# Performance work log

Hardware: AMD Instinct MI355X
Metric: run time of the kernel (lower is better)

Reference implementation:

```python
import jax, jax.numpy as jnp
import numpy as np

DIM = 128
POS_HID = 64
ATTN_MULT = 4
K_NEIGH = 16
B, N = 2, 2048


def setup_inputs() -> dict:
    key = jax.random.key(0)
    ks = jax.random.split(key, 10)
    s = 0.02
    inp = {
        "x": jax.random.normal(ks[0], (B, N, DIM), dtype=jnp.float32),
        "pos": jax.random.normal(ks[1], (B, N, 3), dtype=jnp.float32),
        "mask": jnp.ones((B, N), dtype=bool),
        # to_qkv: Linear(dim, 3*dim, bias=False) -> W (3*dim, dim)
        "Wqkv": jax.random.normal(ks[2], (3 * DIM, DIM), dtype=jnp.float32) * s,
        # pos_mlp: Linear(3, 64) -> ReLU -> Linear(64, dim)
        "Wp1": jax.random.normal(ks[3], (POS_HID, 3), dtype=jnp.float32) * s,
        "bp1": jnp.zeros((POS_HID,), dtype=jnp.float32),
        "Wp2": jax.random.normal(ks[4], (DIM, POS_HID), dtype=jnp.float32) * s,
        "bp2": jnp.zeros((DIM,), dtype=jnp.float32),
        # attn_mlp: Linear(dim, 4*dim) -> ReLU -> Linear(4*dim, dim)
        "Wa1": jax.random.normal(ks[5], (ATTN_MULT * DIM, DIM), dtype=jnp.float32) * s,
        "ba1": jnp.zeros((ATTN_MULT * DIM,), dtype=jnp.float32),
        "Wa2": jax.random.normal(ks[6], (DIM, ATTN_MULT * DIM), dtype=jnp.float32) * s,
        "ba2": jnp.zeros((DIM,), dtype=jnp.float32),
    }
    return inp


def _forward(x, pos, mask, Wqkv, Wp1, bp1, Wp2, bp2, Wa1, ba1, Wa2, ba2):
    b, n, d = x.shape
    qkv = jnp.einsum("bnd,ed->bne", x, Wqkv)  # (b, n, 3*dim)
    q, k, v = jnp.split(qkv, 3, axis=-1)

    # pairwise distances over full n x n for kNN selection
    rel_pos_full = pos[:, :, None, :] - pos[:, None, :, :]  # (b, n, n, 3)
    rel_dist = jnp.linalg.norm(rel_pos_full, axis=-1)        # (b, n, n)
    pair_mask = mask[:, :, None] & mask[:, None, :]
    big = jnp.finfo(rel_dist.dtype).max
    rel_dist = jnp.where(pair_mask, rel_dist, big)

    # topk smallest distances -> neighbor indices (b, n, K)
    _, idx = jax.lax.top_k(-rel_dist, K_NEIGH)

    bi = jnp.arange(b)[:, None, None]
    k_g = k[bi, idx]      # (b, n, K, dim)
    v_g = v[bi, idx]      # (b, n, K, dim)
    pos_g = pos[bi, idx]  # (b, n, K, 3)
    mask_g = jnp.take_along_axis(pair_mask, idx, axis=2)  # (b, n, K)

    # relative position embedding (computed on gathered neighbors; same math
    # as applying pos_mlp on the full n x n tensor then gathering)
    rel_pos = pos[:, :, None, :] - pos_g  # (b, n, K, 3)
    h = jax.nn.relu(jnp.einsum("bnkc,hc->bnkh", rel_pos, Wp1) + bp1)
    rel_pos_emb = jnp.einsum("bnkh,dh->bnkd", h, Wp2) + bp2  # (b, n, K, dim)

    qk_rel = q[:, :, None, :] - k_g  # (b, n, K, dim)
    v_g = v_g + rel_pos_emb

    a = jax.nn.relu(jnp.einsum("bnkd,hd->bnkh", qk_rel + rel_pos_emb, Wa1) + ba1)
    sim = jnp.einsum("bnkh,dh->bnkd", a, Wa2) + ba2  # (b, n, K, dim)

    neg_big = -jnp.finfo(sim.dtype).max
    sim = jnp.where(mask_g[..., None], sim, neg_big)
    attn = jax.nn.softmax(sim, axis=-2)  # softmax over neighbors
    agg = jnp.sum(attn * v_g, axis=2)    # (b, n, dim)
    return agg


def reference(x, pos, mask, Wqkv, Wp1, bp1, Wp2, bp2, Wa1, ba1, Wa2, ba2):
    return _forward(x, pos, mask, Wqkv, Wp1, bp1, Wp2, bp2, Wa1, ba1, Wa2, ba2)
```

## Files before the change

kernel.cpp:

```cpp
#include <hip/hip_runtime.h>
#include <float.h>

#define DIM   128
#define PH    64
#define AH    512
#define KN    16
#define BATCH 2
#define NPTS  2048
#define QB    4
#define RWS   64
#define HC    64
#define NCH   (AH/HC)
#define QR    8
#define KNB   8
#define KBUF  48

#define NB_KNN  (BATCH*NPTS/KNB)
#define NB_QKV  (BATCH*NPTS/QR)
#define NB_CONV 544

typedef __attribute__((ext_vector_type(8))) short bf16x8;
typedef __attribute__((ext_vector_type(4))) float f32x4;

__device__ __forceinline__ unsigned short f2bf(float f) {
    unsigned u = __float_as_uint(f);
    u += 0x7FFFu + ((u >> 16) & 1u);
    return (unsigned short)(u >> 16);
}
__device__ __forceinline__ float bfu(unsigned short u) {
    return __uint_as_float((unsigned)u << 16);
}

__device__ __forceinline__ int yoff(int row, int col) {
    return row * 128 + ((((col >> 3) ^ (row & 7)) << 3) | (col & 7));
}
__device__ __forceinline__ int hoff(int row, int col) {
    return row * 64 + ((((col >> 3) ^ (row & 7)) << 3) | (col & 7));
}

__device__ __forceinline__ unsigned long long bitonic64(unsigned long long key, int lane) {
    #pragma unroll
    for (int k = 2; k <= 64; k <<= 1) {
        #pragma unroll
        for (int j = k >> 1; j > 0; j >>= 1) {
            unsigned long long o = __shfl_xor(key, j);
            bool up  = ((lane & k) == 0);
            bool low = ((lane & j) == 0);
            unsigned long long mn = key < o ? key : o;
            unsigned long long mx = key < o ? o : key;
            key = (up == low) ? mn : mx;
        }
    }
    return key;
}

__device__ __forceinline__ void topk_step(
    unsigned long long key, bool active,
    unsigned long long& lkey, unsigned long long& kmax,
    int& base, unsigned long long* bufw, int lane) {
    unsigned long long m = __ballot(active);
    while (m) {
        int space = KBUF - base;
        int rank  = __popcll(m & ((1ull << lane) - 1ull));
        bool mine = (m >> lane) & 1ull;
        bool app  = mine && (rank < space);
        if (app) bufw[base + rank] = key;
        int cnt = __popcll(m);
        if (cnt <= space) { base += cnt; break; }
        unsigned long long k2 = (lane < KN) ? lkey : bufw[lane - KN];
        k2   = bitonic64(k2, lane);
        lkey = (lane < KN) ? k2 : ~0ull;
        kmax = __shfl(k2, 15);
        base = 0;
        active = active && !app && (key < kmax);
        m = __ballot(active);
    }
}

__global__ __launch_bounds__(256) void front_kernel(
    const float* __restrict__ x, const float* __restrict__ pos,
    const float* __restrict__ Wqkv,
    const float* __restrict__ Wa1, const float* __restrict__ Wa2,
    const float* __restrict__ Wp2,
    float* __restrict__ qkv, int* __restrict__ knn,
    unsigned short* __restrict__ Wa1b, unsigned short* __restrict__ Wa2b,
    unsigned short* __restrict__ Wp2b) {

    __shared__ __align__(16) unsigned char smem[3 * NPTS * 4 + KNB * KBUF * 8];
    int bid = blockIdx.x;
    int t   = threadIdx.x;

    if (bid < NB_KNN) {
        float* lin = (float*)smem;
        unsigned long long (*buf)[KBUF] =
            (unsigned long long(*)[KBUF])(smem + 3 * NPTS * 4);

        int lane = t & 63;
        int wv   = t >> 6;
        int q0   = bid * KNB;
        int b    = q0 >> 11;

        const float* pb = pos + (size_t)b * NPTS * 3;
        for (int i = t; i < 3 * NPTS; i += 256)
            lin[i] = pb[i];
        __syncthreads();

        int qA  = q0 + wv * 2 + 0;
        int qB  = q0 + wv * 2 + 1;
        int iA  = qA & (NPTS - 1), iB = qB & (NPTS - 1);
        float qxA = lin[3 * iA + 0], qyA = lin[3 * iA + 1], qzA = lin[3 * iA + 2];
        float qxB = lin[3 * iB + 0], qyB = lin[3 * iB + 1], qzB = lin[3 * iB + 2];

        unsigned long long lkeyA, lkeyB;
        {
            float cx = lin[3 * lane + 0], cy = lin[3 * lane + 1], cz = lin[3 * lane + 2];
            float dxA = qxA - cx, dyA = qyA - cy, dzA = qzA - cz;
            float dxB = qxB - cx, dyB = qyB - cy, dzB = qzB - cz;
            float d2A = dxA * dxA + dyA * dyA + dzA * dzA;
            float d2B = dxB * dxB + dyB * dyB + dzB * dzB;
            unsigned long long kA =
                ((unsigned long long)__float_as_uint(d2A) << 32) | (unsigned)lane;
            unsigned long long kB =
                ((unsigned long long)__float_as_uint(d2B) << 32) | (unsigned)lane;
            kA = bitonic64(kA, lane);
            kB = bitonic64(kB, lane);
            lkeyA = (lane < KN) ? kA : ~0ull;
            lkeyB = (lane < KN) ? kB : ~0ull;
        }
        unsigned long long kmaxA = __shfl(lkeyA, 15);
        unsigned long long kmaxB = __shfl(lkeyB, 15);
        int baseA = 0, baseB = 0;
        unsigned long long* bufA = buf[wv * 2 + 0];
        unsigned long long* bufB = buf[wv * 2 + 1];

        for (int c = 1; c < NPTS / 64; c++) {
            int j = c * 64 + lane;
            float cx = lin[3 * j + 0], cy = lin[3 * j + 1], cz = lin[3 * j + 2];
            float dxA = qxA - cx, dyA = qyA - cy, dzA = qzA - cz;
            float dxB = qxB - cx, dyB = qyB - cy, dzB = qzB - cz;
            float d2A = dxA * dxA + dyA * dyA + dzA * dzA;
            float d2B = dxB * dxB + dyB * dyB + dzB * dzB;
            unsigned long long kA =
                ((unsigned long long)__float_as_uint(d2A) << 32) | (unsigned)j;
            unsigned long long kB =
                ((unsigned long long)__float_as_uint(d2B) << 32) | (unsigned)j;
            topk_step(kA, kA < kmaxA, lkeyA, kmaxA, baseA, bufA, lane);
            topk_step(kB, kB < kmaxB, lkeyB, kmaxB, baseB, bufB, lane);
        }
        if (baseA) {
            unsigned long long k2 = (lane < KN) ? lkeyA
                : ((lane - KN < baseA) ? bufA[lane - KN] : ~0ull);
            lkeyA = bitonic64(k2, lane);
        }
        if (baseB) {
            unsigned long long k2 = (lane < KN) ? lkeyB
                : ((lane - KN < baseB) ? bufB[lane - KN] : ~0ull);
            lkeyB = bitonic64(k2, lane);
        }
        if (lane < KN) {
            knn[qA * KN + lane] = (int)(unsigned)(lkeyA & 0xFFFFFFFFull);
            knn[qB * KN + lane] = (int)(unsigned)(lkeyB & 0xFFFFFFFFull);
        }
        return;
    }

    if (bid < NB_KNN + NB_QKV) {
        int r0 = (bid - NB_KNN) * QR;
        float (*xr)[DIM] = (float(*)[DIM])smem;
        for (int i = t; i < QR * DIM; i += 256)
            xr[i >> 7][i & 127] = x[(size_t)(r0 + (i >> 7)) * DIM + (i & 127)];
        __syncthreads();
        for (int e = t; e < 3 * DIM; e += 256) {
            const float* wp = Wqkv + e * DIM;
            float a[QR];
            #pragma unroll
            for (int r = 0; r < QR; r++) a[r] = 0.f;
            for (int d = 0; d < DIM; d += 4) {
                float4 wv = *(const float4*)(wp + d);
                #pragma unroll
                for (int r = 0; r < QR; r++) {
                    float4 xv = *(const float4*)&xr[r][d];
                    a[r] += xv.x * wv.x + xv.y * wv.y + xv.z * wv.z + xv.w * wv.w;
                }
            }
            #pragma unroll
            for (int r = 0; r < QR; r++)
                qkv[(size_t)(r0 + r) * 3 * DIM + e] = a[r];
        }
        return;
    }

    {
        int i = (bid - NB_KNN - NB_QKV) * 256 + t;
        if (i < AH * DIM) Wa1b[i] = f2bf(Wa1[i]);
        else if (i < 2 * AH * DIM) Wa2b[i - AH * DIM] = f2bf(Wa2[i - AH * DIM]);
        else if (i < 2 * AH * DIM + DIM * PH) Wp2b[i - 2 * AH * DIM] = f2bf(Wp2[i - 2 * AH * DIM]);
    }
}

__global__ __launch_bounds__(256, 4) void fused_kernel(
    const float* __restrict__ qkv, const float* __restrict__ pos,
    const int* __restrict__ knn,
    const float* __restrict__ Wp1, const float* __restrict__ bp1,
    const float* __restrict__ bp2,
    const unsigned short* __restrict__ Wp2b,
    const unsigned short* __restrict__ Wa1b, const float* __restrict__ ba1,
    const unsigned short* __restrict__ Wa2b, const float* __restrict__ ba2,
    float* __restrict__ out) {

    __shared__ __align__(16) unsigned short Yl[RWS * DIM];
    __shared__ __align__(16) unsigned short Bl[RWS * HC];
    __shared__ __align__(16) unsigned short Vl[RWS * DIM];

    float* qf   = (float*)Bl;
    int*   nid  = (int*)Bl + 512;
    float* relp = (float*)Bl + 576;
    unsigned short* Hh = Vl;

    int t  = threadIdx.x;
    int bid = blockIdx.x;
    int x8 = bid & 7, n8 = bid >> 3;
    int jq = (x8 >> 2) * 512 + n8 * 4 + (x8 & 3);
    int q0 = jq * QB;
    int gb = q0 >> 11;

    for (int i = t; i < QB * DIM; i += 256)
        qf[i] = qkv[(size_t)(q0 + (i >> 7)) * 3 * DIM + (i & 127)];
    if (t < RWS) nid[t] = knn[q0 * KN + t];
    __syncthreads();
    if (t < RWS) {
        int gq = q0 + (t >> 4);
        int gn = (gb << 11) + nid[t];
        relp[t * 3 + 0] = pos[gq * 3 + 0] - pos[gn * 3 + 0];
        relp[t * 3 + 1] = pos[gq * 3 + 1] - pos[gn * 3 + 1];
        relp[t * 3 + 2] = pos[gq * 3 + 2] - pos[gn * 3 + 2];
    }
    __syncthreads();

    for (int i = t; i < RWS * PH; i += 256) {
        int row = i >> 6, h = i & 63;
        float hv = relp[row * 3 + 0] * Wp1[h * 3 + 0]
                 + relp[row * 3 + 1] * Wp1[h * 3 + 1]
                 + relp[row * 3 + 2] * Wp1[h * 3 + 2] + bp1[h];
        Hh[hoff(row, h)] = f2bf(fmaxf(hv, 0.f));
    }
    __syncthreads();

    int w = t >> 6, lane = t & 63, lg = lane >> 4, lr = lane & 15;

    f32x4 emb[4][2];
    #pragma unroll
    for (int mi = 0; mi < 4; mi++)
        #pragma unroll
        for (int ni = 0; ni < 2; ni++) {
            float bz = bp2[w * 32 + ni * 16 + lr];
            emb[mi][ni] = (f32x4){bz, bz, bz, bz};
        }
    #pragma unroll
    for (int kk = 0; kk < 2; kk++) {
        bf16x8 bfr[2];
        #pragma unroll
        for (int ni = 0; ni < 2; ni++)
            bfr[ni] = *(const bf16x8*)(Wp2b + (w * 32 + ni * 16 + lr) * PH + kk * 32 + lg * 8);
        #pragma unroll
        for (int mi = 0; mi < 4; mi++) {
            bf16x8 afr = *(const bf16x8*)&Hh[hoff(mi * 16 + lr, kk * 32 + lg * 8)];
            #pragma unroll
            for (int ni = 0; ni < 2; ni++)
                emb[mi][ni] = __builtin_amdgcn_mfma_f32_16x16x32_bf16(afr, bfr[ni], emb[mi][ni], 0, 0, 0);
        }
    }

    #pragma unroll
    for (int mi = 0; mi < 4; mi++)
        #pragma unroll
        for (int ni = 0; ni < 2; ni++) {
            int colb = w * 32 + ni * 16 + lr;
            #pragma unroll
            for (int r = 0; r < 4; r++)
                Yl[yoff(mi * 16 + lg * 4 + r, colb)] = f2bf(emb[mi][ni][r]);
        }
    __syncthreads();

    for (int i = t; i < RWS * 32; i += 256) {
        int row = i >> 5, cg = (i & 31) * 4;
        const float* kvp = qkv + (size_t)((gb << 11) + nid[row]) * 3 * DIM;
        float4 kg = *(const float4*)(kvp + DIM + cg);
        float4 vg = *(const float4*)(kvp + 2 * DIM + cg);
        float4 qv = *(const float4*)(qf + (row >> 4) * DIM + cg);
        int off = yoff(row, cg);
        ushort4 em = *(const ushort4*)&Yl[off];
        float e0 = bfu(em.x), e1 = bfu(em.y), e2 = bfu(em.z), e3 = bfu(em.w);
        ushort4 yv, vv;
        yv.x = f2bf(qv.x - kg.x + e0); yv.y = f2bf(qv.y - kg.y + e1);
        yv.z = f2bf(qv.z - kg.z + e2); yv.w = f2bf(qv.w - kg.w + e3);
        vv.x = f2bf(vg.x + e0); vv.y = f2bf(vg.y + e1);
        vv.z = f2bf(vg.z + e2); vv.w = f2bf(vg.w + e3);
        *(ushort4*)&Yl[off] = yv;
        *(ushort4*)&Vl[off] = vv;
    }
    __syncthreads();

    f32x4 sim[4][2];
    #pragma unroll
    for (int mi = 0; mi < 4; mi++)
        #pragma unroll
        for (int ni = 0; ni < 2; ni++) {
            float bz = ba2[w * 32 + ni * 16 + lr];
            sim[mi][ni] = (f32x4){bz, bz, bz, bz};
        }

    #pragma unroll 2
    for (int ch = 0; ch < NCH; ch++) {
        bf16x8 w1f[4], w2f[4];
        #pragma unroll
        for (int kk = 0; kk < 4; kk++)
            w1f[kk] = *(const bf16x8*)(Wa1b + (ch * HC + w * 16 + lr) * DIM + kk * 32 + lg * 8);
        #pragma unroll
        for (int i = 0; i < 4; i++) {
            int kk = i >> 1, ni = i & 1;
            w2f[i] = *(const bf16x8*)(Wa2b + (w * 32 + ni * 16 + lr) * AH + ch * HC + kk * 32 + lg * 8);
        }

        f32x4 ac[4];
        float bz = ba1[ch * HC + w * 16 + lr];
        #pragma unroll
        for (int mi = 0; mi < 4; mi++) ac[mi] = (f32x4){bz, bz, bz, bz};
        #pragma unroll
        for (int kk = 0; kk < 4; kk++)
            #pragma unroll
            for (int mi = 0; mi < 4; mi++) {
                bf16x8 afr = *(const bf16x8*)&Yl[yoff(mi * 16 + lr, kk * 32 + lg * 8)];
                ac[mi] = __builtin_amdgcn_mfma_f32_16x16x32_bf16(afr, w1f[kk], ac[mi], 0, 0, 0);
            }
        #pragma unroll
        for (int mi = 0; mi < 4; mi++)
            #pragma unroll
            for (int r = 0; r < 4; r++)
                Bl[hoff(mi * 16 + lg * 4 + r, w * 16 + lr)] = f2bf(fmaxf(ac[mi][r], 0.f));
        __syncthreads();

        #pragma unroll
        for (int kk = 0; kk < 2; kk++)
            #pragma unroll
            for (int mi = 0; mi < 4; mi++) {
                bf16x8 afr = *(const bf16x8*)&Bl[hoff(mi * 16 + lr, kk * 32 + lg * 8)];
                #pragma unroll
                for (int ni = 0; ni < 2; ni++)
                    sim[mi][ni] = __builtin_amdgcn_mfma_f32_16x16x32_bf16(afr, w2f[kk * 2 + ni], sim[mi][ni], 0, 0, 0);
            }
        __syncthreads();
    }

    #pragma unroll
    for (int mi = 0; mi < 4; mi++) {
        #pragma unroll
        for (int ni = 0; ni < 2; ni++) {
            int colb = w * 32 + ni * 16 + lr;
            int rw   = mi * 16 + lg * 4;
            float s0 = sim[mi][ni][0], s1 = sim[mi][ni][1];
            float s2 = sim[mi][ni][2], s3 = sim[mi][ni][3];
            float m = fmaxf(fmaxf(s0, s1), fmaxf(s2, s3));
            m = fmaxf(m, __shfl_xor(m, 16));
            m = fmaxf(m, __shfl_xor(m, 32));
            float e0 = __expf(s0 - m), e1 = __expf(s1 - m);
            float e2 = __expf(s2 - m), e3 = __expf(s3 - m);
            float v0 = bfu(Vl[yoff(rw + 0, colb)]);
            float v1 = bfu(Vl[yoff(rw + 1, colb)]);
            float v2 = bfu(Vl[yoff(rw + 2, colb)]);
            float v3 = bfu(Vl[yoff(rw + 3, colb)]);
            float ssum = (e0 + e1) + (e2 + e3);
            float wsum = (e0 * v0 + e1 * v1) + (e2 * v2 + e3 * v3);
            ssum += __shfl_xor(ssum, 16);
            ssum += __shfl_xor(ssum, 32);
            wsum += __shfl_xor(wsum, 16);
            wsum += __shfl_xor(wsum, 32);
            if (lg == 0)
                out[(size_t)(q0 + mi) * DIM + colb] = wsum / ssum;
        }
    }
}

extern "C" void kernel_launch(void* const* d_in, const int* in_sizes, int n_in,
                              void* d_out, int out_size, void* d_ws, size_t ws_size,
                              hipStream_t stream) {
    const float* x    = (const float*)d_in[0];
    const float* pos  = (const float*)d_in[1];
    const float* Wqkv = (const float*)d_in[3];
    const float* Wp1  = (const float*)d_in[4];
    const float* bp1  = (const float*)d_in[5];
    const float* Wp2  = (const float*)d_in[6];
    const float* bp2  = (const float*)d_in[7];
    const float* Wa1  = (const float*)d_in[8];
    const float* ba1  = (const float*)d_in[9];
    const float* Wa2  = (const float*)d_in[10];
    const float* ba2  = (const float*)d_in[11];
    float* out = (float*)d_out;

    char* ws = (char*)d_ws;
    float* qkv = (float*)ws;                              ws += (size_t)BATCH * NPTS * 3 * DIM * 4;
    int*   knn = (int*)ws;                                ws += (size_t)BATCH * NPTS * KN * 4;
    unsigned short* Wa1b = (unsigned short*)ws;           ws += AH * DIM * 2;
    unsigned short* Wa2b = (unsigned short*)ws;           ws += AH * DIM * 2;
    unsigned short* Wp2b = (unsigned short*)ws;           ws += DIM * PH * 2;

    front_kernel<<<NB_KNN + NB_QKV + NB_CONV, 256, 0, stream>>>(
        x, pos, Wqkv, Wa1, Wa2, Wp2, qkv, knn, Wa1b, Wa2b, Wp2b);
    fused_kernel<<<BATCH * NPTS / QB, 256, 0, stream>>>(qkv, pos, knn,
                                                        Wp1, bp1, bp2, Wp2b,
                                                        Wa1b, ba1, Wa2b, ba2, out);
}
```

Measured before the change: 78.49 us.

## Partition attention MLP by query rows per wave, removing block barriers

Each wave now owns one query's 16 neighbor rows and computes the full hidden and output width for them, instead of all waves splitting the output columns across all rows. The Y fragments are kept in registers, and the Bl hidden tile is written and read only by the same wave, so both __syncthreads per chunk go away. The cost is that every wave loads the whole Wa1/Wa2 chunk itself, so per-wave weight traffic from global/L2 rises, and sim accumulators grow to 8 tiles per wave.

Result: slower. 155.4 us (+98.1%).

```diff
diff --git a/kernel.cpp b/kernel.cpp
--- a/kernel.cpp
+++ b/kernel.cpp
@@ -301,83 +301,76 @@
     }
     __syncthreads();
 
-    f32x4 sim[4][2];
-    #pragma unroll
-    for (int mi = 0; mi < 4; mi++)
-        #pragma unroll
-        for (int ni = 0; ni < 2; ni++) {
-            float bz = ba2[w * 32 + ni * 16 + lr];
-            sim[mi][ni] = (f32x4){bz, bz, bz, bz};
-        }
-
-    #pragma unroll 2
+    bf16x8 yreg[4];
+    #pragma unroll
+    for (int kk = 0; kk < 4; kk++)
+        yreg[kk] = *(const bf16x8*)&Yl[yoff(w * 16 + lr, kk * 32 + lg * 8)];
+
+    f32x4 sim[8];
+    #pragma unroll
+    for (int ni = 0; ni < 8; ni++) {
+        float bz = ba2[ni * 16 + lr];
+        sim[ni] = (f32x4){bz, bz, bz, bz};
+    }
+
     for (int ch = 0; ch < NCH; ch++) {
-        bf16x8 w1f[4], w2f[4];
-        #pragma unroll
-        for (int kk = 0; kk < 4; kk++)
-            w1f[kk] = *(const bf16x8*)(Wa1b + (ch * HC + w * 16 + lr) * DIM + kk * 32 + lg * 8);
-        #pragma unroll
-        for (int i = 0; i < 4; i++) {
-            int kk = i >> 1, ni = i & 1;
-            w2f[i] = *(const bf16x8*)(Wa2b + (w * 32 + ni * 16 + lr) * AH + ch * HC + kk * 32 + lg * 8);
-        }
-
         f32x4 ac[4];
-        float bz = ba1[ch * HC + w * 16 + lr];
-        #pragma unroll
-        for (int mi = 0; mi < 4; mi++) ac[mi] = (f32x4){bz, bz, bz, bz};
-        #pragma unroll
-        for (int kk = 0; kk < 4; kk++)
-            #pragma unroll
-            for (int mi = 0; mi < 4; mi++) {
-                bf16x8 afr = *(const bf16x8*)&Yl[yoff(mi * 16 + lr, kk * 32 + lg * 8)];
-                ac[mi] = __builtin_amdgcn_mfma_f32_16x16x32_bf16(afr, w1f[kk], ac[mi], 0, 0, 0);
+        #pragma unroll
+        for (int ni = 0; ni < 4; ni++) {
+            float b1 = ba1[ch * HC + ni * 16 + lr];
+            ac[ni] = (f32x4){b1, b1, b1, b1};
+        }
+        #pragma unroll
+        for (int kk = 0; kk < 4; kk++) {
+            bf16x8 w1a = *(const bf16x8*)(Wa1b + (size_t)(ch * HC + 0 * 16 + lr) * DIM + kk * 32 + lg * 8);
+            bf16x8 w1b = *(const bf16x8*)(Wa1b + (size_t)(ch * HC + 1 * 16 + lr) * DIM + kk * 32 + lg * 8);
+            bf16x8 w1c = *(const bf16x8*)(Wa1b + (size_t)(ch * HC + 2 * 16 + lr) * DIM + kk * 32 + lg * 8);
+            bf16x8 w1d = *(const bf16x8*)(Wa1b + (size_t)(ch * HC + 3 * 16 + lr) * DIM + kk * 32 + lg * 8);
+            ac[0] = __builtin_amdgcn_mfma_f32_16x16x32_bf16(yreg[kk], w1a, ac[0], 0, 0, 0);
+            ac[1] = __builtin_amdgcn_mfma_f32_16x16x32_bf16(yreg[kk], w1b, ac[1], 0, 0, 0);
+            ac[2] = __builtin_amdgcn_mfma_f32_16x16x32_bf16(yreg[kk], w1c, ac[2], 0, 0, 0);
+            ac[3] = __builtin_amdgcn_mfma_f32_16x16x32_bf16(yreg[kk], w1d, ac[3], 0, 0, 0);
+        }
+        #pragma unroll
+        for (int ni = 0; ni < 4; ni++)
+            #pragma unroll
+            for (int r = 0; r < 4; r++)
+                Bl[hoff(w * 16 + lg * 4 + r, ni * 16 + lr)] = f2bf(fmaxf(ac[ni][r], 0.f));
+
+        #pragma unroll
+        for (int kk = 0; kk < 2; kk++) {
+            bf16x8 afr = *(const bf16x8*)&Bl[hoff(w * 16 + lr, kk * 32 + lg * 8)];
+            #pragma unroll
+            for (int ni = 0; ni < 8; ni++) {
+                bf16x8 w2 = *(const bf16x8*)(Wa2b + (size_t)(ni * 16 + lr) * AH + ch * HC + kk * 32 + lg * 8);
+                sim[ni] = __builtin_amdgcn_mfma_f32_16x16x32_bf16(afr, w2, sim[ni], 0, 0, 0);
             }
-        #pragma unroll
-        for (int mi = 0; mi < 4; mi++)
-            #pragma unroll
-            for (int r = 0; r < 4; r++)
-                Bl[hoff(mi * 16 + lg * 4 + r, w * 16 + lr)] = f2bf(fmaxf(ac[mi][r], 0.f));
-        __syncthreads();
-
-        #pragma unroll
-        for (int kk = 0; kk < 2; kk++)
-            #pragma unroll
-            for (int mi = 0; mi < 4; mi++) {
-                bf16x8 afr = *(const bf16x8*)&Bl[hoff(mi * 16 + lr, kk * 32 + lg * 8)];
-                #pragma unroll
-                for (int ni = 0; ni < 2; ni++)
-                    sim[mi][ni] = __builtin_amdgcn_mfma_f32_16x16x32_bf16(afr, w2f[kk * 2 + ni], sim[mi][ni], 0, 0, 0);
-            }
-        __syncthreads();
-    }
-
-    #pragma unroll
-    for (int mi = 0; mi < 4; mi++) {
-        #pragma unroll
-        for (int ni = 0; ni < 2; ni++) {
-            int colb = w * 32 + ni * 16 + lr;
-            int rw   = mi * 16 + lg * 4;
-            float s0 = sim[mi][ni][0], s1 = sim[mi][ni][1];
-            float s2 = sim[mi][ni][2], s3 = sim[mi][ni][3];
-            float m = fmaxf(fmaxf(s0, s1), fmaxf(s2, s3));
-            m = fmaxf(m, __shfl_xor(m, 16));
-            m = fmaxf(m, __shfl_xor(m, 32));
-            float e0 = __expf(s0 - m), e1 = __expf(s1 - m);
-            float e2 = __expf(s2 - m), e3 = __expf(s3 - m);
-            float v0 = bfu(Vl[yoff(rw + 0, colb)]);
-            float v1 = bfu(Vl[yoff(rw + 1, colb)]);
-            float v2 = bfu(Vl[yoff(rw + 2, colb)]);
-            float v3 = bfu(Vl[yoff(rw + 3, colb)]);
-            float ssum = (e0 + e1) + (e2 + e3);
-            float wsum = (e0 * v0 + e1 * v1) + (e2 * v2 + e3 * v3);
-            ssum += __shfl_xor(ssum, 16);
-            ssum += __shfl_xor(ssum, 32);
-            wsum += __shfl_xor(wsum, 16);
-            wsum += __shfl_xor(wsum, 32);
-            if (lg == 0)
-                out[(size_t)(q0 + mi) * DIM + colb] = wsum / ssum;
-        }
+        }
+    }
+
+    #pragma unroll
+    for (int ni = 0; ni < 8; ni++) {
+        int colb = ni * 16 + lr;
+        int rw   = w * 16 + lg * 4;
+        float s0 = sim[ni][0], s1 = sim[ni][1];
+        float s2 = sim[ni][2], s3 = sim[ni][3];
+        float m = fmaxf(fmaxf(s0, s1), fmaxf(s2, s3));
+        m = fmaxf(m, __shfl_xor(m, 16));
+        m = fmaxf(m, __shfl_xor(m, 32));
+        float e0 = __expf(s0 - m), e1 = __expf(s1 - m);
+        float e2 = __expf(s2 - m), e3 = __expf(s3 - m);
+        float v0 = bfu(Vl[yoff(rw + 0, colb)]);
+        float v1 = bfu(Vl[yoff(rw + 1, colb)]);
+        float v2 = bfu(Vl[yoff(rw + 2, colb)]);
+        float v3 = bfu(Vl[yoff(rw + 3, colb)]);
+        float ssum = (e0 + e1) + (e2 + e3);
+        float wsum = (e0 * v0 + e1 * v1) + (e2 * v2 + e3 * v3);
+        ssum += __shfl_xor(ssum, 16);
+        ssum += __shfl_xor(ssum, 32);
+        wsum += __shfl_xor(wsum, 16);
+        wsum += __shfl_xor(wsum, 32);
+        if (lg == 0)
+            out[(size_t)(q0 + w) * DIM + colb] = wsum / ssum;
     }
 }
 
```
